# Optimization experiments

Measured on AMD Instinct MI355X. Metric: run time of the kernel, lower is better.

The kernel has to match this reference:

```python
import jax, jax.numpy as jnp
import numpy as np

B, L, D, H, N = 8, 2048, 128, 4, 2
DK = D // H          # 32
DFF = 2 * D          # 256 (dff = d * 2 in source)


def _init_proj(key, shape):
    # matches torch init: uniform in [-s, s], s = sqrt(6/(fan_in+fan_out)) of last two dims
    s = np.sqrt(6.0 / (shape[-1] + shape[-2]))
    return jax.random.uniform(key, shape, jnp.float32, -s, s)


def setup_inputs() -> dict:
    key = jax.random.key(0)
    ks = jax.random.split(key, 8)
    x = jax.random.normal(ks[0], (B, L, D), jnp.float32)
    mask = jnp.ones((B, L), jnp.float32)
    Wq = _init_proj(ks[1], (N, H, D, DK))
    Wk = _init_proj(ks[2], (N, H, D, DK))
    Wv = _init_proj(ks[3], (N, H, D, DK))
    Wo = _init_proj(ks[4], (N, H * DK, D))
    W1 = _init_proj(ks[5], (N, D, DFF))
    b1 = jnp.zeros((N, 1, 1, DFF), jnp.float32)
    W2 = _init_proj(ks[6], (N, DFF, D))
    b2 = jnp.zeros((N, 1, 1, D), jnp.float32)
    return {"x": x, "mask": mask, "Wq": Wq, "Wk": Wk, "Wv": Wv,
            "Wo": Wo, "W1": W1, "b1": b1, "W2": W2, "b2": b2}


def reference(x, mask, Wq, Wk, Wv, Wo, W1, b1, W2, b2):
    # Eval-mode forward (no attention dropout-mask trick, no FFN dropout).
    neg = jnp.finfo(x.dtype).min
    m2 = mask[:, :, None] * mask[:, None, :]              # [B, L, L]
    add_mask = (1.0 - m2)[:, None, :, :] * neg            # [B, 1, L, L]
    bsz, max_len, _ = x.shape
    for i in range(N):  # small fixed layer loop
        q = jnp.einsum('bld,hde->bhle', x, Wq[i])         # [B,H,L,DK]
        k = jnp.einsum('bld,hde->bhle', x, Wk[i])
        v = jnp.einsum('bld,hde->bhle', x, Wv[i])
        A = jnp.einsum('bhqe,bhke->bhqk', q, k) + add_mask  # note: no 1/sqrt(dk), as in source
        A = jax.nn.softmax(A, axis=-1)                    # [B,H,L,L]
        o = jnp.einsum('bhqk,bhke->bqhe', A, v)           # [B,L,H,DK]
        o = o.reshape(bsz, max_len, H * DK) @ Wo[i]       # [B,L,D]
        x = (o + x) / 2
        f = jax.nn.gelu(x @ W1[i] + b1[i], approximate=False)  # torch F.gelu is exact erf
        f = f @ W2[i] + b2[i]
        x = (f + x) / 2
    return x
```

## Files before the change

kernel.cpp:

```cpp
#include <hip/hip_runtime.h>
#include <math.h>

#define BB 8
#define LL 2048
#define DD 128
#define HH 4
#define DKK 32
#define DFFF 256

#define NEGMIN (-3.402823466e38f)
#define LOG2E 1.44269504088896f

typedef _Float16 f16;
typedef _Float16 f16x4 __attribute__((ext_vector_type(4)));
typedef _Float16 f16x8 __attribute__((ext_vector_type(8)));
typedef __fp16 h16x2 __attribute__((ext_vector_type(2)));
typedef float f32x4 __attribute__((ext_vector_type(4)));

union PKU { h16x2 h2[2]; f16x4 v; };

__global__ __launch_bounds__(256) void setup_kernel(
    const float* __restrict__ x, const float* __restrict__ mask,
    const float* __restrict__ Wq, const float* __restrict__ Wk,
    const float* __restrict__ Wv, const float* __restrict__ Wo,
    const float* __restrict__ W1, const float* __restrict__ W2,
    f16* __restrict__ wt, f16* __restrict__ xh, int* __restrict__ flags) {
  const int blk = blockIdx.x;
  const int t = threadIdx.x;
  if (blk < 1024) {
    const int idx = blk * 256 + t;
    const int i = idx >> 17;
    const int r = idx & 131071;
    float val;
    if (r < 49152) {
      const int sel = r / 16384;
      const int rr = r & 16383;
      const int n = rr >> 7, k = rr & 127;
      const float* W = (sel == 0) ? Wq : (sel == 1) ? Wk : Wv;
      val = W[((size_t)(i * 4 + (n >> 5)) * 128 + k) * 32 + (n & 31)];
    } else if (r < 65536) {
      const int r2 = r - 49152;
      const int n = r2 >> 7, k = r2 & 127;
      val = Wo[i * 16384 + k * 128 + n];
    } else if (r < 98304) {
      const int r2 = r - 65536;
      const int n = r2 >> 7, k = r2 & 127;
      val = W1[i * 32768 + k * 256 + n];
    } else {
      const int r2 = r - 98304;
      const int n = r2 >> 8, k = r2 & 255;
      val = W2[i * 32768 + k * 128 + n];
    }
    wt[idx] = (f16)val;
  } else if (blk < 2048) {
    const int i = ((blk - 1024) * 256 + t) * 8;
    float4 v0 = *(const float4*)(x + i);
    float4 v1 = *(const float4*)(x + i + 4);
    f16x8 h;
    h[0] = (f16)v0.x; h[1] = (f16)v0.y; h[2] = (f16)v0.z; h[3] = (f16)v0.w;
    h[4] = (f16)v1.x; h[5] = (f16)v1.y; h[6] = (f16)v1.z; h[7] = (f16)v1.w;
    *(f16x8*)(xh + i) = h;
  } else {
    __shared__ int wok[4];
    const int b = blk - 2048;
    bool ok = true;
    for (int i = t; i < LL; i += 256) ok &= (mask[b * LL + i] == 1.f);
    const bool all_ok = __all(ok);
    if ((t & 63) == 0) wok[t >> 6] = all_ok ? 1 : 0;
    __syncthreads();
    if (t == 0) flags[b] = wok[0] & wok[1] & wok[2] & wok[3];
  }
}

__global__ __launch_bounds__(256) void qkv_kernel(
    const f16* __restrict__ xh, const f16* __restrict__ wqkvT,
    f16* __restrict__ qh, f16* __restrict__ kh, f16* __restrict__ vth) {
  const int t = threadIdx.x;
  const int wave = t >> 6, lane = t & 63;
  const int g = lane >> 4, c = lane & 15;
  const int rgrp = wave >> 1, half = wave & 1;
  const int r0g = blockIdx.x * 32 + rgrp * 16;
  const int b4 = (r0g >> 11) * 4;
  const int l0 = r0g & 2047;

  f16x8 a[4];
#pragma unroll
  for (int kt = 0; kt < 4; ++kt)
    a[kt] = *(const f16x8*)(xh + (size_t)(r0g + c) * 128 + kt * 32 + g * 8);

  {
    const f16* wT = wqkvT + half * 16384;
    f16* out = (half == 0) ? qh : kh;
#pragma unroll
    for (int nt = 0; nt < 8; ++nt) {
      f32x4 acc = {0.f, 0.f, 0.f, 0.f};
#pragma unroll
      for (int kt = 0; kt < 4; ++kt) {
        f16x8 bfrag = *(const f16x8*)(wT + (nt * 16 + c) * 128 + kt * 32 + g * 8);
        acc = __builtin_amdgcn_mfma_f32_16x16x32_f16(a[kt], bfrag, acc, 0, 0, 0);
      }
      const int h = nt >> 1, e = (nt & 1) * 16 + c;
#pragma unroll
      for (int r = 0; r < 4; ++r)
        out[((size_t)(b4 + h) * LL + l0 + 4 * g + r) * DKK + e] = (f16)acc[r];
    }
  }
  {
    const f16* wT = wqkvT + 2 * 16384;
#pragma unroll
    for (int nt = 0; nt < 4; ++nt) {
      const int ntg = half * 4 + nt;
      f32x4 acc = {0.f, 0.f, 0.f, 0.f};
#pragma unroll
      for (int kt = 0; kt < 4; ++kt) {
        f16x8 afrag = *(const f16x8*)(wT + (ntg * 16 + c) * 128 + kt * 32 + g * 8);
        acc = __builtin_amdgcn_mfma_f32_16x16x32_f16(afrag, a[kt], acc, 0, 0, 0);
      }
#pragma unroll
      for (int r = 0; r < 4; ++r) {
        const int eg = ntg * 16 + 4 * g + r;
        vth[((size_t)(b4 + (eg >> 5)) * DKK + (eg & 31)) * LL + l0 + c] =
            (f16)acc[r];
      }
    }
  }
}

__global__ __launch_bounds__(256, 4) void attn_kernel(
    const f16* __restrict__ qh, const f16* __restrict__ kh,
    const f16* __restrict__ vth, const float* __restrict__ mask,
    const int* __restrict__ bflags, f16* __restrict__ o) {
  __shared__ f16 Vt[4][2][32][72];
  const int t = threadIdx.x;
  const int wave = t >> 6, lane = t & 63;
  const int g = lane >> 4, c = lane & 15;

  const int flat = blockIdx.x;
  const int xcd = flat & 7, slot = flat >> 3;
  const int bh = xcd * 4 + (slot >> 4);
  const int qb = slot & 15;
  const int b = bh >> 2;
  const int qw = qb * 128 + wave * 32;
  const bool nomask_b = (bflags[b] != 0);

  f16x8 qfrag[2];
  float mqv[2] = {1.f, 1.f};
#pragma unroll
  for (int qt = 0; qt < 2; ++qt)
    qfrag[qt] =
        *(const f16x8*)(qh + ((size_t)bh * LL + qw + qt * 16 + c) * DKK + g * 8);
  if (!nomask_b) {
#pragma unroll
    for (int qt = 0; qt < 2; ++qt) mqv[qt] = mask[b * LL + qw + qt * 16 + c];
  }

  f32x4 o4[2][2];
  float m[2], l[2];
#pragma unroll
  for (int qt = 0; qt < 2; ++qt) {
    m[qt] = -3.0e38f; l[qt] = 0.f;
#pragma unroll
    for (int dt = 0; dt < 2; ++dt)
#pragma unroll
      for (int r = 0; r < 4; ++r) o4[qt][dt][r] = 0.f;
  }

  const f16* kp = kh + (size_t)bh * LL * DKK + (size_t)c * DKK + g * 8;
  const int vd = lane >> 3, vseg = lane & 7;
  const f16* vp = vth + (size_t)bh * DKK * LL + (size_t)vd * LL + vseg * 8;

#define LOADK(DST, KT)                                       \
  {                                                          \
    const f16* _p = kp + (size_t)(KT) * 64 * DKK;            \
    DST[0] = *(const f16x8*)(_p);                            \
    DST[1] = *(const f16x8*)(_p + 16 * DKK);                 \
    DST[2] = *(const f16x8*)(_p + 32 * DKK);                 \
    DST[3] = *(const f16x8*)(_p + 48 * DKK);                 \
  }
#define LOADVREG(DST, KT)                                    \
  {                                                          \
    const f16* _p = vp + (KT) * 64;                          \
    DST[0] = *(const f16x8*)(_p);                            \
    DST[1] = *(const f16x8*)(_p + 8 * LL);                   \
    DST[2] = *(const f16x8*)(_p + 16 * LL);                  \
    DST[3] = *(const f16x8*)(_p + 24 * LL);                  \
  }
#define COMMITV(SRC, BUF)                                    \
  {                                                          \
    *(f16x8*)&Vt[wave][BUF][vd][vseg * 8] = SRC[0];          \
    *(f16x8*)&Vt[wave][BUF][vd + 8][vseg * 8] = SRC[1];      \
    *(f16x8*)&Vt[wave][BUF][vd + 16][vseg * 8] = SRC[2];     \
    *(f16x8*)&Vt[wave][BUF][vd + 24][vseg * 8] = SRC[3];     \
  }

  f16x8 kbA[4], kbB[4], vr[4];

  LOADVREG(vr, 0);
  LOADK(kbA, 0);
  COMMITV(vr, 0);

  for (int kt = 0; kt < 32; ++kt) {
    const int cur = kt & 1;
    if (kt < 31) {
      LOADK(kbB, kt + 1);
      LOADVREG(vr, kt + 1);
    }

    f32x4 st[2][4];
    __builtin_amdgcn_s_setprio(1);
#pragma unroll
    for (int qt = 0; qt < 2; ++qt)
#pragma unroll
      for (int nt = 0; nt < 4; ++nt) {
        f32x4 z = {0.f, 0.f, 0.f, 0.f};
        st[qt][nt] =
            __builtin_amdgcn_mfma_f32_16x16x32_f16(kbA[nt], qfrag[qt], z, 0, 0, 0);
      }
    __builtin_amdgcn_s_setprio(0);

    if (!nomask_b) {
      const int k0 = kt * 64;
#pragma unroll
      for (int qt = 0; qt < 2; ++qt) {
        const float mq = mqv[qt];
#pragma unroll
        for (int nt = 0; nt < 4; ++nt) {
          float4 mk4 = *(const float4*)(mask + b * LL + k0 + nt * 16 + 4 * g);
          st[qt][nt][0] += (1.f - mq * mk4.x) * NEGMIN;
          st[qt][nt][1] += (1.f - mq * mk4.y) * NEGMIN;
          st[qt][nt][2] += (1.f - mq * mk4.z) * NEGMIN;
          st[qt][nt][3] += (1.f - mq * mk4.w) * NEGMIN;
        }
      }
    }

    f16x4 va[2][4];
#pragma unroll
    for (int dt = 0; dt < 2; ++dt)
#pragma unroll
      for (int nt = 0; nt < 4; ++nt)
        va[dt][nt] = *(const f16x4*)&Vt[wave][cur][dt * 16 + c][nt * 16 + 4 * g];

#pragma unroll
    for (int qt = 0; qt < 2; ++qt) {
      float vml = fmaxf(fmaxf(st[qt][0][0], st[qt][0][1]),
                        fmaxf(st[qt][0][2], st[qt][0][3]));
#pragma unroll
      for (int nt = 1; nt < 4; ++nt)
        vml = fmaxf(vml, fmaxf(fmaxf(st[qt][nt][0], st[qt][nt][1]),
                               fmaxf(st[qt][nt][2], st[qt][nt][3])));

      if (!__all(vml - m[qt] <= 8.f)) {
        float vm = fmaxf(vml, __shfl_xor(vml, 16));
        vm = fmaxf(vm, __shfl_xor(vm, 32));
        const float mn = fmaxf(m[qt], vm);
        const float sc = __builtin_exp2f((m[qt] - mn) * LOG2E);
        l[qt] *= sc;
#pragma unroll
        for (int dt = 0; dt < 2; ++dt)
#pragma unroll
          for (int r = 0; r < 4; ++r) o4[qt][dt][r] *= sc;
        m[qt] = mn;
      }
      const float mn2 = m[qt] * LOG2E;

      float p[4][4];
      float psum = 0.f;
#pragma unroll
      for (int nt = 0; nt < 4; ++nt) {
#pragma unroll
        for (int r = 0; r < 4; ++r) {
          p[nt][r] = __builtin_exp2f(fmaf(st[qt][nt][r], LOG2E, -mn2));
          psum += p[nt][r];
        }
      }
      l[qt] += psum;

      __builtin_amdgcn_s_setprio(1);
#pragma unroll
      for (int nt = 0; nt < 4; ++nt) {
        PKU pk;
        pk.h2[0] = __builtin_amdgcn_cvt_pkrtz(p[nt][0], p[nt][1]);
        pk.h2[1] = __builtin_amdgcn_cvt_pkrtz(p[nt][2], p[nt][3]);
        o4[qt][0] = __builtin_amdgcn_mfma_f32_16x16x16f16(va[0][nt], pk.v,
                                                          o4[qt][0], 0, 0, 0);
        o4[qt][1] = __builtin_amdgcn_mfma_f32_16x16x16f16(va[1][nt], pk.v,
                                                          o4[qt][1], 0, 0, 0);
      }
      __builtin_amdgcn_s_setprio(0);
    }

    if (kt < 31) {
      COMMITV(vr, 1 - cur);
#pragma unroll
      for (int i = 0; i < 4; ++i) kbA[i] = kbB[i];
    }
  }
#undef LOADK
#undef LOADVREG
#undef COMMITV

  const int h = bh & 3;
#pragma unroll
  for (int qt = 0; qt < 2; ++qt) {
    float lt = l[qt];
    lt += __shfl_xor(lt, 16);
    lt += __shfl_xor(lt, 32);
    const float rdiv = 1.f / lt;
    f16* orow = o + ((size_t)b * LL + qw + qt * 16 + c) * DD + h * DKK;
#pragma unroll
    for (int dt = 0; dt < 2; ++dt) {
      f16x4 res;
      res[0] = (f16)(o4[qt][dt][0] * rdiv);
      res[1] = (f16)(o4[qt][dt][1] * rdiv);
      res[2] = (f16)(o4[qt][dt][2] * rdiv);
      res[3] = (f16)(o4[qt][dt][3] * rdiv);
      *(f16x4*)(orow + dt * 16 + g * 4) = res;
    }
  }
}

__global__ __launch_bounds__(256) void mlp_kernel(
    const f16* __restrict__ o, const float* __restrict__ x,
    const f16* __restrict__ WoT, const f16* __restrict__ W1T,
    const f16* __restrict__ W2T, const float* __restrict__ b1,
    const float* __restrict__ b2, float* __restrict__ xout,
    const f16* __restrict__ wqkvT_next,
    f16* __restrict__ qh, f16* __restrict__ kh, f16* __restrict__ vth) {
  __shared__ f16 Xm[32][136];
  __shared__ f16 Fs[32][264];
  const int t = threadIdx.x;
  const int wave = t >> 6, lane = t & 63;
  const int g = lane >> 4, c = lane & 15;
  const int rgrp = wave >> 1, half = wave & 1;
  const int mrow = rgrp * 16;
  const long r0 = (long)blockIdx.x * 32;

  f16x8 a1[4];
#pragma unroll
  for (int kt = 0; kt < 4; ++kt)
    a1[kt] = *(const f16x8*)(o + (r0 + mrow + c) * 128 + kt * 32 + g * 8);

  f32x4 xmreg[4];
#pragma unroll
  for (int nt = 0; nt < 4; ++nt) {
    const int ntg = half * 4 + nt;
    f32x4 acc = {0.f, 0.f, 0.f, 0.f};
#pragma unroll
    for (int kt = 0; kt < 4; ++kt) {
      f16x8 bfrag = *(const f16x8*)(WoT + (ntg * 16 + c) * 128 + kt * 32 + g * 8);
      acc = __builtin_amdgcn_mfma_f32_16x16x32_f16(a1[kt], bfrag, acc, 0, 0, 0);
    }
#pragma unroll
    for (int r = 0; r < 4; ++r) {
      const float xv = x[(r0 + mrow + 4 * g + r) * 128 + ntg * 16 + c];
      acc[r] = (acc[r] + xv) * 0.5f;
      Xm[mrow + 4 * g + r][ntg * 16 + c] = (f16)acc[r];
    }
    xmreg[nt] = acc;
  }
  __syncthreads();

  f16x8 a2[4];
#pragma unroll
  for (int kt = 0; kt < 4; ++kt)
    a2[kt] = *(const f16x8*)&Xm[mrow + c][kt * 32 + g * 8];
#pragma unroll
  for (int nt = 0; nt < 8; ++nt) {
    const int ntg = half * 8 + nt;
    f32x4 acc = {0.f, 0.f, 0.f, 0.f};
#pragma unroll
    for (int kt = 0; kt < 4; ++kt) {
      f16x8 bfrag = *(const f16x8*)(W1T + (ntg * 16 + c) * 128 + kt * 32 + g * 8);
      acc = __builtin_amdgcn_mfma_f32_16x16x32_f16(a2[kt], bfrag, acc, 0, 0, 0);
    }
    const float bj = b1[ntg * 16 + c];
#pragma unroll
    for (int r = 0; r < 4; ++r) {
      const float val = acc[r] + bj;
      Fs[mrow + 4 * g + r][ntg * 16 + c] =
          (f16)(0.5f * val * (1.f + erff(val * 0.70710678118654752f)));
    }
  }
  __syncthreads();

  f16x8 a3[8];
#pragma unroll
  for (int kt = 0; kt < 8; ++kt)
    a3[kt] = *(const f16x8*)&Fs[mrow + c][kt * 32 + g * 8];
#pragma unroll
  for (int nt = 0; nt < 4; ++nt) {
    const int ntg = half * 4 + nt;
    f32x4 acc = {0.f, 0.f, 0.f, 0.f};
#pragma unroll
    for (int kt = 0; kt < 8; ++kt) {
      f16x8 bfrag = *(const f16x8*)(W2T + (ntg * 16 + c) * 256 + kt * 32 + g * 8);
      acc = __builtin_amdgcn_mfma_f32_16x16x32_f16(a3[kt], bfrag, acc, 0, 0, 0);
    }
    const float bj = b2[ntg * 16 + c];
#pragma unroll
    for (int r = 0; r < 4; ++r) {
      const float val = (acc[r] + bj + xmreg[nt][r]) * 0.5f;
      xout[(r0 + mrow + 4 * g + r) * 128 + ntg * 16 + c] = val;
      Xm[mrow + 4 * g + r][ntg * 16 + c] = (f16)val;
    }
  }

  if (wqkvT_next) {
    __syncthreads();
    const int r0g = (int)r0 + mrow;
    const int b4 = (r0g >> 11) * 4;
    const int l0 = r0g & 2047;
    f16x8 a[4];
#pragma unroll
    for (int kt = 0; kt < 4; ++kt)
      a[kt] = *(const f16x8*)&Xm[mrow + c][kt * 32 + g * 8];

    {
      const f16* wT = wqkvT_next + half * 16384;
      f16* out = (half == 0) ? qh : kh;
#pragma unroll
      for (int nt = 0; nt < 8; ++nt) {
        f32x4 acc = {0.f, 0.f, 0.f, 0.f};
#pragma unroll
        for (int kt = 0; kt < 4; ++kt) {
          f16x8 bfrag =
              *(const f16x8*)(wT + (nt * 16 + c) * 128 + kt * 32 + g * 8);
          acc = __builtin_amdgcn_mfma_f32_16x16x32_f16(a[kt], bfrag, acc, 0, 0, 0);
        }
        const int h = nt >> 1, e = (nt & 1) * 16 + c;
#pragma unroll
        for (int r = 0; r < 4; ++r)
          out[((size_t)(b4 + h) * LL + l0 + 4 * g + r) * DKK + e] = (f16)acc[r];
      }
    }
    {
      const f16* wT = wqkvT_next + 2 * 16384;
#pragma unroll
      for (int nt = 0; nt < 4; ++nt) {
        const int ntg = half * 4 + nt;
        f32x4 acc = {0.f, 0.f, 0.f, 0.f};
#pragma unroll
        for (int kt = 0; kt < 4; ++kt) {
          f16x8 afrag =
              *(const f16x8*)(wT + (ntg * 16 + c) * 128 + kt * 32 + g * 8);
          acc = __builtin_amdgcn_mfma_f32_16x16x32_f16(afrag, a[kt], acc, 0, 0, 0);
        }
#pragma unroll
        for (int r = 0; r < 4; ++r) {
          const int eg = ntg * 16 + 4 * g + r;
          vth[((size_t)(b4 + (eg >> 5)) * DKK + (eg & 31)) * LL + l0 + c] =
              (f16)acc[r];
        }
      }
    }
  }
}

extern "C" void kernel_launch(void* const* d_in, const int* in_sizes, int n_in,
                              void* d_out, int out_size, void* d_ws,
                              size_t ws_size, hipStream_t stream) {
  const float* x    = (const float*)d_in[0];
  const float* mask = (const float*)d_in[1];
  const float* Wq   = (const float*)d_in[2];
  const float* Wk   = (const float*)d_in[3];
  const float* Wv   = (const float*)d_in[4];
  const float* Wo   = (const float*)d_in[5];
  const float* W1   = (const float*)d_in[6];
  const float* b1   = (const float*)d_in[7];
  const float* W2   = (const float*)d_in[8];
  const float* b2   = (const float*)d_in[9];

  const size_t SZ = (size_t)BB * LL * DD;
  char* p = (char*)d_ws;
  f16* qh   = (f16*)p;  p += SZ * sizeof(f16);
  f16* kh   = (f16*)p;  p += SZ * sizeof(f16);
  f16* vth  = (f16*)p;  p += SZ * sizeof(f16);
  f16* ob   = (f16*)p;  p += SZ * sizeof(f16);
  f16* xh0  = (f16*)p;  p += SZ * sizeof(f16);
  f16* wt   = (f16*)p;  p += (size_t)262144 * sizeof(f16);
  int* bflags = (int*)p; p += 256;
  float* xA = (float*)p;

  setup_kernel<<<2056, 256, 0, stream>>>(x, mask, Wq, Wk, Wv, Wo, W1, W2,
                                         wt, xh0, bflags);

  for (int i = 0; i < 2; ++i) {
    const float* xin = (i == 0) ? x : xA;
    float* xout = (i == 1) ? (float*)d_out : xA;
    const f16* qkvT_i = wt + (size_t)i * 131072;
    const f16* WoT_i  = wt + (size_t)i * 131072 + 49152;
    const f16* W1T_i  = wt + (size_t)i * 131072 + 65536;
    const f16* W2T_i  = wt + (size_t)i * 131072 + 98304;
    const float* b1_i = b1 + (long)i * DFFF;
    const float* b2_i = b2 + (long)i * DD;
    const f16* qkvT_next = (i == 0) ? (wt + 131072) : nullptr;

    if (i == 0)
      qkv_kernel<<<(BB * LL) / 32, 256, 0, stream>>>(xh0, qkvT_i, qh, kh, vth);
    attn_kernel<<<512, 256, 0, stream>>>(qh, kh, vth, mask, bflags, ob);
    mlp_kernel<<<(BB * LL) / 32, 256, 0, stream>>>(ob, xin, WoT_i, W1T_i, W2T_i,
                                                   b1_i, b2_i, xout,
                                                   qkvT_next, qh, kh, vth);
  }
}
```

Baseline: 197.9 us.

## Split attention KV range across two wave groups and merge partial softmax states

The attention block doubles from 4 to 8 waves. Each pair of waves shares a query group, and each wave in the pair handles half of the key/value sequence, flash-decoding style. The second half writes its partial O, running max and row sum to shared memory, and the first half merges them with rescaling before writing the output. This shortens each wave's serial loop and raises the number of waves in flight across the 512 blocks. The cost is the extra merge step, a block barrier, more LDS per block, and possible occupancy limits from the 512-thread blocks.

New measurement: 201.5 us. Within noise of the previous version (+1.8%).

```diff
diff --git a/kernel.cpp b/kernel.cpp
--- a/kernel.cpp
+++ b/kernel.cpp
@@ -126,21 +126,23 @@
   }
 }
 
-__global__ __launch_bounds__(256, 4) void attn_kernel(
+__global__ __launch_bounds__(512, 4) void attn_kernel(
     const f16* __restrict__ qh, const f16* __restrict__ kh,
     const f16* __restrict__ vth, const float* __restrict__ mask,
     const int* __restrict__ bflags, f16* __restrict__ o) {
-  __shared__ f16 Vt[4][2][32][72];
+  __shared__ f16 Vt[8][2][32][72];
   const int t = threadIdx.x;
   const int wave = t >> 6, lane = t & 63;
   const int g = lane >> 4, c = lane & 15;
+  const int qgrp = wave & 3, z = wave >> 2;
 
   const int flat = blockIdx.x;
   const int xcd = flat & 7, slot = flat >> 3;
   const int bh = xcd * 4 + (slot >> 4);
   const int qb = slot & 15;
   const int b = bh >> 2;
-  const int qw = qb * 128 + wave * 32;
+  const int qw = qb * 128 + qgrp * 32;
+  const int kv0 = z * (LL / 2);
   const bool nomask_b = (bflags[b] != 0);
 
   f16x8 qfrag[2];
@@ -165,9 +167,11 @@
       for (int r = 0; r < 4; ++r) o4[qt][dt][r] = 0.f;
   }
 
-  const f16* kp = kh + (size_t)bh * LL * DKK + (size_t)c * DKK + g * 8;
+  const f16* kp = kh + (size_t)bh * LL * DKK + (size_t)kv0 * DKK +
+                  (size_t)c * DKK + g * 8;
   const int vd = lane >> 3, vseg = lane & 7;
-  const f16* vp = vth + (size_t)bh * DKK * LL + (size_t)vd * LL + vseg * 8;
+  const f16* vp = vth + (size_t)bh * DKK * LL + (size_t)vd * LL + kv0 +
+                  vseg * 8;
 
 #define LOADK(DST, KT)                                       \
   {                                                          \
@@ -199,9 +203,9 @@
   LOADK(kbA, 0);
   COMMITV(vr, 0);
 
-  for (int kt = 0; kt < 32; ++kt) {
+  for (int kt = 0; kt < 16; ++kt) {
     const int cur = kt & 1;
-    if (kt < 31) {
+    if (kt < 15) {
       LOADK(kbB, kt + 1);
       LOADVREG(vr, kt + 1);
     }
@@ -212,14 +216,14 @@
     for (int qt = 0; qt < 2; ++qt)
 #pragma unroll
       for (int nt = 0; nt < 4; ++nt) {
-        f32x4 z = {0.f, 0.f, 0.f, 0.f};
+        f32x4 zz = {0.f, 0.f, 0.f, 0.f};
         st[qt][nt] =
-            __builtin_amdgcn_mfma_f32_16x16x32_f16(kbA[nt], qfrag[qt], z, 0, 0, 0);
+            __builtin_amdgcn_mfma_f32_16x16x32_f16(kbA[nt], qfrag[qt], zz, 0, 0, 0);
       }
     __builtin_amdgcn_s_setprio(0);
 
     if (!nomask_b) {
-      const int k0 = kt * 64;
+      const int k0 = kv0 + kt * 64;
 #pragma unroll
       for (int qt = 0; qt < 2; ++qt) {
         const float mq = mqv[qt];
@@ -290,7 +294,7 @@
       __builtin_amdgcn_s_setprio(0);
     }
 
-    if (kt < 31) {
+    if (kt < 15) {
       COMMITV(vr, 1 - cur);
 #pragma unroll
       for (int i = 0; i < 4; ++i) kbA[i] = kbB[i];
@@ -300,22 +304,48 @@
 #undef LOADVREG
 #undef COMMITV
 
-  const int h = bh & 3;
-#pragma unroll
-  for (int qt = 0; qt < 2; ++qt) {
-    float lt = l[qt];
-    lt += __shfl_xor(lt, 16);
-    lt += __shfl_xor(lt, 32);
-    const float rdiv = 1.f / lt;
-    f16* orow = o + ((size_t)b * LL + qw + qt * 16 + c) * DD + h * DKK;
-#pragma unroll
-    for (int dt = 0; dt < 2; ++dt) {
-      f16x4 res;
-      res[0] = (f16)(o4[qt][dt][0] * rdiv);
-      res[1] = (f16)(o4[qt][dt][1] * rdiv);
-      res[2] = (f16)(o4[qt][dt][2] * rdiv);
-      res[3] = (f16)(o4[qt][dt][3] * rdiv);
-      *(f16x4*)(orow + dt * 16 + g * 4) = res;
+  if (z == 1) {
+    float* pl = (float*)&Vt[wave][0][0][0] + lane * 20;
+    *(f32x4*)(pl + 0) = o4[0][0];
+    *(f32x4*)(pl + 4) = o4[0][1];
+    *(f32x4*)(pl + 8) = o4[1][0];
+    *(f32x4*)(pl + 12) = o4[1][1];
+    f32x4 mlv;
+    mlv[0] = m[0]; mlv[1] = m[1]; mlv[2] = l[0]; mlv[3] = l[1];
+    *(f32x4*)(pl + 16) = mlv;
+  }
+  __syncthreads();
+  if (z == 1) return;
+
+  {
+    const float* pl = (const float*)&Vt[wave + 4][0][0][0] + lane * 20;
+    f32x4 po[2][2];
+    po[0][0] = *(const f32x4*)(pl + 0);
+    po[0][1] = *(const f32x4*)(pl + 4);
+    po[1][0] = *(const f32x4*)(pl + 8);
+    po[1][1] = *(const f32x4*)(pl + 12);
+    const f32x4 mlv = *(const f32x4*)(pl + 16);
+
+    const int h = bh & 3;
+#pragma unroll
+    for (int qt = 0; qt < 2; ++qt) {
+      const float M = fmaxf(m[qt], mlv[qt]);
+      const float w0 = __builtin_exp2f((m[qt] - M) * LOG2E);
+      const float w1 = __builtin_exp2f((mlv[qt] - M) * LOG2E);
+      float lt = w0 * l[qt] + w1 * mlv[2 + qt];
+      lt += __shfl_xor(lt, 16);
+      lt += __shfl_xor(lt, 32);
+      const float rdiv = 1.f / lt;
+      f16* orow = o + ((size_t)b * LL + qw + qt * 16 + c) * DD + h * DKK;
+#pragma unroll
+      for (int dt = 0; dt < 2; ++dt) {
+        f16x4 res;
+        res[0] = (f16)((w0 * o4[qt][dt][0] + w1 * po[qt][dt][0]) * rdiv);
+        res[1] = (f16)((w0 * o4[qt][dt][1] + w1 * po[qt][dt][1]) * rdiv);
+        res[2] = (f16)((w0 * o4[qt][dt][2] + w1 * po[qt][dt][2]) * rdiv);
+        res[3] = (f16)((w0 * o4[qt][dt][3] + w1 * po[qt][dt][3]) * rdiv);
+        *(f16x4*)(orow + dt * 16 + g * 4) = res;
+      }
     }
   }
 }
@@ -498,7 +528,7 @@
 
     if (i == 0)
       qkv_kernel<<<(BB * LL) / 32, 256, 0, stream>>>(xh0, qkvT_i, qh, kh, vth);
-    attn_kernel<<<512, 256, 0, stream>>>(qh, kh, vth, mask, bflags, ob);
+    attn_kernel<<<512, 512, 0, stream>>>(qh, kh, vth, mask, bflags, ob);
     mlp_kernel<<<(BB * LL) / 32, 256, 0, stream>>>(ob, xin, WoT_i, W1T_i, W2T_i,
                                                    b1_i, b2_i, xout,
                                                    qkvT_next, qh, kh, vth);
```
